# Kernel optimization log

Hardware: AMD Instinct MI355X
Metric: run time of the kernel (lower is better)

The kernel has to match this reference:

```python
import jax, jax.numpy as jnp
import numpy as np

NUM_HEADS = 16


def setup_inputs() -> dict:
    key = jax.random.key(0)
    k0, k1, k2, k3 = jax.random.split(key, 4)
    S, dim = 8192, 1280              # packed vision tokens, embed dim
    H = NUM_HEADS
    D = dim // H                      # head_dim = 80
    n_seg = 8                         # 8 images x 1024 patches
    L = S // n_seg
    return {
        "hidden_states": jax.random.normal(k0, (S, dim), jnp.float32),
        "rotary_pos_emb": jax.random.normal(k1, (S, D // 2), jnp.float32),
        "w_qkv": jax.random.normal(k2, (3 * dim, dim), jnp.float32) * 0.02,
        "b_qkv": jnp.zeros((3 * dim,), jnp.float32),
        "w_proj": jax.random.normal(k3, (dim, dim), jnp.float32) * 0.02,
        "b_proj": jnp.zeros((dim,), jnp.float32),
        "cu_seqlens": jnp.arange(n_seg + 1, dtype=jnp.int32) * L,
    }


def _rotate_half(x):
    x1, x2 = jnp.split(x, 2, axis=-1)
    return jnp.concatenate([-x2, x1], axis=-1)


def _apply_rope(t, freqs):
    # t: [S, H, D]; freqs: [S, D//2]. Matches cat+rotate_half formulation
    # (cos/sin repeated to full head_dim), computed in float32.
    emb = jnp.concatenate([freqs, freqs], axis=-1)          # [S, D]
    cos = jnp.cos(emb)[:, None, :]                          # [S, 1, D]
    sin = jnp.sin(emb)[:, None, :]
    return t * cos + _rotate_half(t) * sin


def reference(hidden_states, rotary_pos_emb, w_qkv, b_qkv, w_proj, b_proj, cu_seqlens):
    S, dim = hidden_states.shape
    H = NUM_HEADS
    D = dim // H
    n_seg = cu_seqlens.shape[0] - 1   # equal-length packed segments
    L = S // n_seg

    qkv = hidden_states @ w_qkv.T + b_qkv                   # [S, 3*dim]
    q, k, v = jnp.split(qkv, 3, axis=-1)
    q = q.reshape(S, H, D)
    k = k.reshape(S, H, D)
    v = v.reshape(S, H, D)

    q = _apply_rope(q, rotary_pos_emb)
    k = _apply_rope(k, rotary_pos_emb)

    # block-diagonal varlen attention: batch over segments instead of an
    # [S, S] dense mask (honors the cu_seqlens sparsity structure)
    qs = q.reshape(n_seg, L, H, D)
    ks = k.reshape(n_seg, L, H, D)
    vs = v.reshape(n_seg, L, H, D)
    scale = D ** -0.5
    scores = jnp.einsum('blhd,bthd->bhlt', qs, ks) * scale  # [n_seg, H, L, L]
    probs = jax.nn.softmax(scores, axis=-1)
    ctx = jnp.einsum('bhlt,bthd->blhd', probs, vs)          # [n_seg, L, H, D]
    ctx = ctx.reshape(S, dim)

    return ctx @ w_proj.T + b_proj                          # [S, dim]
```

## Files before the change

### kernel.cpp

```cpp
#include <hip/hip_runtime.h>
#include <hip/hip_bf16.h>
#include <math.h>

#define S_TOK   8192
#define DIM     1280
#define NHEAD   16
#define HDIM    80
#define NSEG    8
#define SEGLEN  1024
#define QKV_LD  3840
#define DPAD    96

typedef __attribute__((ext_vector_type(8))) short bf16x8;
typedef __attribute__((ext_vector_type(4))) float f32x4;

__device__ __forceinline__ short f2b(float x) {
  __hip_bfloat16 h = __float2bfloat16(x);
  return *reinterpret_cast<short*>(&h);
}
__device__ __forceinline__ float b2f(short x) {
  __hip_bfloat16 h;
  *reinterpret_cast<short*>(&h) = x;
  return __bfloat162float(h);
}

__device__ __forceinline__ void gl_lds16(const void* g, void* l) {
  __builtin_amdgcn_global_load_lds(
      (const __attribute__((address_space(1))) unsigned int*)g,
      (__attribute__((address_space(3))) unsigned int*)l, 16, 0, 0);
}

__global__ __launch_bounds__(256) void cast_f32_bf16(
    const float* __restrict__ in, short* __restrict__ out, int n4)
{
  const int i = blockIdx.x * 256 + threadIdx.x;
  if (i >= n4) return;
  const float4 v = ((const float4*)in)[i];
  short4 o;
  o.x = f2b(v.x); o.y = f2b(v.y); o.z = f2b(v.z); o.w = f2b(v.w);
  ((short4*)out)[i] = o;
}

template<bool OUT_BF16>
__global__ __launch_bounds__(256) void gemm_mfma_nt(
    const short* __restrict__ A, const short* __restrict__ B,
    const float* __restrict__ bias, void* __restrict__ Cout,
    int M, int N, int K)
{
  __shared__ short As[128 * 32];
  __shared__ short Bs[128 * 32];
  const int t = threadIdx.x;
  const int wave = t >> 6, lane = t & 63;
  const int q = lane >> 4, r = lane & 15;
  const int bm = blockIdx.y * 128, bn = blockIdx.x * 128;
  const int wr = (wave >> 1) * 64, wc = (wave & 1) * 64;

  f32x4 acc[4][4];
#pragma unroll
  for (int i = 0; i < 4; ++i)
#pragma unroll
    for (int j = 0; j < 4; ++j) acc[i][j] = (f32x4)(0.f);

  for (int k0 = 0; k0 < K; k0 += 32) {
    __syncthreads();
#pragma unroll
    for (int i = 0; i < 2; ++i) {
      const int c = i * 256 + t;
      const int row = c >> 2, off = (c & 3) * 8;
      gl_lds16(A + (size_t)(bm + row) * K + k0 + off, As + c * 8);
      gl_lds16(B + (size_t)(bn + row) * K + k0 + off, Bs + c * 8);
    }
    __syncthreads();

    bf16x8 af[4], bg[4];
#pragma unroll
    for (int mt = 0; mt < 4; ++mt)
      af[mt] = *(const bf16x8*)&As[(wr + mt * 16 + r) * 32 + q * 8];
#pragma unroll
    for (int nt = 0; nt < 4; ++nt)
      bg[nt] = *(const bf16x8*)&Bs[(wc + nt * 16 + r) * 32 + q * 8];
#pragma unroll
    for (int mt = 0; mt < 4; ++mt)
#pragma unroll
      for (int nt = 0; nt < 4; ++nt)
        acc[mt][nt] = __builtin_amdgcn_mfma_f32_16x16x32_bf16(
            af[mt], bg[nt], acc[mt][nt], 0, 0, 0);
  }

#pragma unroll
  for (int mt = 0; mt < 4; ++mt)
#pragma unroll
    for (int nt = 0; nt < 4; ++nt)
#pragma unroll
      for (int reg = 0; reg < 4; ++reg) {
        const int mrow = bm + wr + mt * 16 + q * 4 + reg;
        const int ncol = bn + wc + nt * 16 + r;
        const float v = acc[mt][nt][reg] + bias[ncol];
        if (OUT_BF16)
          ((short*)Cout)[(size_t)mrow * N + ncol] = f2b(v);
        else
          ((float*)Cout)[(size_t)mrow * N + ncol] = v;
      }
}

__global__ __launch_bounds__(256) void rope_cast(
    const short* __restrict__ qkvb, const float* __restrict__ rot,
    short* __restrict__ Qb, short* __restrict__ Kb)
{
  const int idx = blockIdx.x * 256 + threadIdx.x;
  const int j = idx % 48;
  const int h = (idx / 48) % NHEAD;
  const int s = idx / (48 * NHEAD);
  short* qo = Qb + ((size_t)s * NHEAD + h) * DPAD;
  short* ko = Kb + ((size_t)s * NHEAD + h) * DPAD;
  if (j < 40) {
    const float f = rot[s * 40 + j];
    const float c = cosf(f), sn = sinf(f);
    const short* qi = qkvb + (size_t)s * QKV_LD + h * HDIM;
    const short* ki = qi + DIM;
    const float scale = 0.11180339887498949f;
    const float q0 = b2f(qi[j]), q1 = b2f(qi[j + 40]);
    qo[j]      = f2b((q0 * c - q1 * sn) * scale);
    qo[j + 40] = f2b((q1 * c + q0 * sn) * scale);
    const float k0 = b2f(ki[j]), k1 = b2f(ki[j + 40]);
    ko[j]      = f2b(k0 * c - k1 * sn);
    ko[j + 40] = f2b(k1 * c + k0 * sn);
  } else {
    const int z = 80 + (j - 40);
    qo[z] = 0; qo[z + 8] = 0;
    ko[z] = 0; ko[z + 8] = 0;
  }
}

#define LQK 104
#define LVT 72
#define LPR 72

__global__ __launch_bounds__(256) void attn_mfma(
    const short* __restrict__ Qb, const short* __restrict__ Kb,
    const short* __restrict__ qkvb, short* __restrict__ ctxb)
{
  __shared__ short Qs[64 * LQK];
  __shared__ short Ks[64 * LQK];
  __shared__ short Vt[80 * LVT];
  __shared__ short Ps[4][16 * LPR];

  const int t = threadIdx.x;
  const int wave = t >> 6, lane = t & 63;
  const int q = lane >> 4, r = lane & 15;
  const int seg = blockIdx.z, head = blockIdx.y;
  const int m0 = blockIdx.x * 64;
  const size_t srow0 = (size_t)seg * SEGLEN;

#pragma unroll
  for (int i = 0; i < 3; ++i) {
    const int c = i * 256 + t;
    const int row = c / 12, off = (c % 12) * 8;
    *(bf16x8*)&Qs[row * LQK + off] =
        *(const bf16x8*)(Qb + ((srow0 + m0 + row) * NHEAD + head) * DPAD + off);
  }
  __syncthreads();
  bf16x8 qf[3];
#pragma unroll
  for (int ks = 0; ks < 3; ++ks)
    qf[ks] = *(const bf16x8*)&Qs[(wave * 16 + r) * LQK + ks * 32 + q * 8];

  float m_[4], l_[4];
  f32x4 o[5];
#pragma unroll
  for (int i = 0; i < 4; ++i) { m_[i] = -1e30f; l_[i] = 0.f; }
#pragma unroll
  for (int i = 0; i < 5; ++i) o[i] = (f32x4)(0.f);

  for (int n0 = 0; n0 < SEGLEN; n0 += 64) {
    __syncthreads();
#pragma unroll
    for (int i = 0; i < 3; ++i) {
      const int c = i * 256 + t;
      const int row = c / 12, off = (c % 12) * 8;
      *(bf16x8*)&Ks[row * LQK + off] =
          *(const bf16x8*)(Kb + ((srow0 + n0 + row) * NHEAD + head) * DPAD + off);
    }
#pragma unroll
    for (int i = 0; i < 3; ++i) {
      const int c = i * 256 + t;
      if (c < 640) {
        const int kv = c / 10, c0 = (c % 10) * 8;
        bf16x8 v = *(const bf16x8*)(qkvb + (srow0 + n0 + kv) * QKV_LD +
                                    2 * DIM + head * HDIM + c0);
#pragma unroll
        for (int jj = 0; jj < 8; ++jj)
          Vt[(c0 + jj) * LVT + kv] = v[jj];
      }
    }
    __syncthreads();

    f32x4 s[4];
#pragma unroll
    for (int nt = 0; nt < 4; ++nt) s[nt] = (f32x4)(0.f);
#pragma unroll
    for (int ks = 0; ks < 3; ++ks)
#pragma unroll
      for (int nt = 0; nt < 4; ++nt) {
        bf16x8 kf = *(const bf16x8*)&Ks[(nt * 16 + r) * LQK + ks * 32 + q * 8];
        s[nt] = __builtin_amdgcn_mfma_f32_16x16x32_bf16(qf[ks], kf, s[nt], 0, 0, 0);
      }

#pragma unroll
    for (int reg = 0; reg < 4; ++reg) {
      float sm = fmaxf(fmaxf(s[0][reg], s[1][reg]), fmaxf(s[2][reg], s[3][reg]));
#pragma unroll
      for (int off = 1; off < 16; off <<= 1)
        sm = fmaxf(sm, __shfl_xor(sm, off));
      const float mn = fmaxf(m_[reg], sm);
      const float corr = __expf(m_[reg] - mn);
      m_[reg] = mn;
      float ps = 0.f;
#pragma unroll
      for (int nt = 0; nt < 4; ++nt) {
        const float e = __expf(s[nt][reg] - mn);
        s[nt][reg] = e;
        ps += e;
      }
#pragma unroll
      for (int off = 1; off < 16; off <<= 1)
        ps += __shfl_xor(ps, off);
      l_[reg] = l_[reg] * corr + ps;
#pragma unroll
      for (int dt = 0; dt < 5; ++dt) o[dt][reg] *= corr;
    }

#pragma unroll
    for (int nt = 0; nt < 4; ++nt)
#pragma unroll
      for (int reg = 0; reg < 4; ++reg)
        Ps[wave][(q * 4 + reg) * LPR + nt * 16 + r] = f2b(s[nt][reg]);

#pragma unroll
    for (int ks2 = 0; ks2 < 2; ++ks2) {
      bf16x8 pf = *(const bf16x8*)&Ps[wave][r * LPR + ks2 * 32 + q * 8];
#pragma unroll
      for (int dt = 0; dt < 5; ++dt) {
        bf16x8 vf = *(const bf16x8*)&Vt[(dt * 16 + r) * LVT + ks2 * 32 + q * 8];
        o[dt] = __builtin_amdgcn_mfma_f32_16x16x32_bf16(pf, vf, o[dt], 0, 0, 0);
      }
    }
  }

#pragma unroll
  for (int reg = 0; reg < 4; ++reg) {
    const float inv = 1.f / l_[reg];
    const size_t row = srow0 + m0 + wave * 16 + q * 4 + reg;
#pragma unroll
    for (int dt = 0; dt < 5; ++dt)
      ctxb[row * DIM + head * HDIM + dt * 16 + r] = f2b(o[dt][reg] * inv);
  }
}

extern "C" void kernel_launch(void* const* d_in, const int* in_sizes, int n_in,
                              void* d_out, int out_size, void* d_ws, size_t ws_size,
                              hipStream_t stream)
{
  const float* hs    = (const float*)d_in[0];
  const float* rot   = (const float*)d_in[1];
  const float* wqkv  = (const float*)d_in[2];
  const float* bqkv  = (const float*)d_in[3];
  const float* wproj = (const float*)d_in[4];
  const float* bproj = (const float*)d_in[5];
  float* out = (float*)d_out;

  char* w = (char*)d_ws;
  short* hs_b    = (short*)w;  w += (size_t)S_TOK * DIM * 2;
  short* wqkv_b  = (short*)w;  w += (size_t)QKV_LD * DIM * 2;
  short* wproj_b = (short*)w;  w += (size_t)DIM * DIM * 2;
  short* qkv_b   = (short*)w;  w += (size_t)S_TOK * QKV_LD * 2;
  short* Qb      = (short*)w;  w += (size_t)S_TOK * NHEAD * DPAD * 2;
  short* Kb      = (short*)w;  w += (size_t)S_TOK * NHEAD * DPAD * 2;
  short* ctx_b   = (short*)w;  w += (size_t)S_TOK * DIM * 2;

  dim3 blk(256);

  cast_f32_bf16<<<dim3(S_TOK * DIM / 4 / 256), blk, 0, stream>>>(hs, hs_b, S_TOK * DIM / 4);
  cast_f32_bf16<<<dim3(QKV_LD * DIM / 4 / 256), blk, 0, stream>>>(wqkv, wqkv_b, QKV_LD * DIM / 4);
  cast_f32_bf16<<<dim3(DIM * DIM / 4 / 256), blk, 0, stream>>>(wproj, wproj_b, DIM * DIM / 4);

  gemm_mfma_nt<true><<<dim3(QKV_LD / 128, S_TOK / 128), blk, 0, stream>>>(
      hs_b, wqkv_b, bqkv, qkv_b, S_TOK, QKV_LD, DIM);

  rope_cast<<<dim3(S_TOK * NHEAD * 48 / 256), blk, 0, stream>>>(qkv_b, rot, Qb, Kb);

  attn_mfma<<<dim3(SEGLEN / 64, NHEAD, NSEG), blk, 0, stream>>>(Qb, Kb, qkv_b, ctx_b);

  gemm_mfma_nt<false><<<dim3(DIM / 128, S_TOK / 128), blk, 0, stream>>>(
      ctx_b, wproj_b, bproj, out, S_TOK, DIM, DIM);
}
```

Baseline: 533.7 us.

## Pre-transpose V globally, prefetch K/V into registers, 128-row Q tiles per block

Adds a separate kernel that writes V transposed per segment/head into the reused hidden-states workspace, so attention loads V tiles with vector stores instead of scattered per-element LDS transposes. The attention kernel now processes 32 query rows per wave (128 per block), keeping Q fragments in registers and reusing each K/V tile across two M tiles. The next K/V tile is prefetched into registers while the current one is computed, and MFMA sections get raised wave priority. Costs are an extra launch plus a global V round trip, higher register pressure with a launch-bound occupancy hint of 3, and half as many blocks.

```diff
diff --git a/kernel.cpp b/kernel.cpp
--- a/kernel.cpp
+++ b/kernel.cpp
@@ -132,129 +132,177 @@
   }
 }
 
+__global__ __launch_bounds__(256) void v_transpose(
+    const short* __restrict__ qkvb, short* __restrict__ Vt)
+{
+  const int tid = blockIdx.x * 256 + threadIdx.x;
+  const int c   = tid >> 13;
+  const int kv  = tid & 8191;
+  const int head = c / 10;
+  const int d0   = (c % 10) * 8;
+  const int seg  = kv >> 10;
+  const bf16x8 v = *(const bf16x8*)(qkvb + (size_t)kv * QKV_LD + 2 * DIM +
+                                    head * HDIM + d0);
+  short* ob = Vt + ((size_t)(seg * NHEAD + head) * HDIM + d0) * SEGLEN + (kv & 1023);
+#pragma unroll
+  for (int j = 0; j < 8; ++j)
+    ob[(size_t)j * SEGLEN] = v[j];
+}
+
 #define LQK 104
 #define LVT 72
 #define LPR 72
-
-__global__ __launch_bounds__(256) void attn_mfma(
+#define NT  16
+
+__global__ __launch_bounds__(256, 3) void attn_mfma(
     const short* __restrict__ Qb, const short* __restrict__ Kb,
-    const short* __restrict__ qkvb, short* __restrict__ ctxb)
-{
-  __shared__ short Qs[64 * LQK];
+    const short* __restrict__ Vtg, short* __restrict__ ctxb)
+{
   __shared__ short Ks[64 * LQK];
-  __shared__ short Vt[80 * LVT];
-  __shared__ short Ps[4][16 * LPR];
+  __shared__ short Vs[80 * LVT];
+  __shared__ short Ps[4][32 * LPR];
 
   const int t = threadIdx.x;
   const int wave = t >> 6, lane = t & 63;
   const int q = lane >> 4, r = lane & 15;
   const int seg = blockIdx.z, head = blockIdx.y;
-  const int m0 = blockIdx.x * 64;
+  const int m0 = blockIdx.x * 128;
   const size_t srow0 = (size_t)seg * SEGLEN;
-
-#pragma unroll
-  for (int i = 0; i < 3; ++i) {
-    const int c = i * 256 + t;
-    const int row = c / 12, off = (c % 12) * 8;
-    *(bf16x8*)&Qs[row * LQK + off] =
-        *(const bf16x8*)(Qb + ((srow0 + m0 + row) * NHEAD + head) * DPAD + off);
-  }
-  __syncthreads();
-  bf16x8 qf[3];
-#pragma unroll
-  for (int ks = 0; ks < 3; ++ks)
-    qf[ks] = *(const bf16x8*)&Qs[(wave * 16 + r) * LQK + ks * 32 + q * 8];
-
-  float m_[4], l_[4];
-  f32x4 o[5];
-#pragma unroll
-  for (int i = 0; i < 4; ++i) { m_[i] = -1e30f; l_[i] = 0.f; }
-#pragma unroll
-  for (int i = 0; i < 5; ++i) o[i] = (f32x4)(0.f);
-
-  for (int n0 = 0; n0 < SEGLEN; n0 += 64) {
+  const size_t vbase = (size_t)(seg * NHEAD + head) * HDIM * SEGLEN;
+
+  bf16x8 qf[2][3];
+#pragma unroll
+  for (int mt = 0; mt < 2; ++mt)
+#pragma unroll
+    for (int ks = 0; ks < 3; ++ks)
+      qf[mt][ks] = *(const bf16x8*)(
+          Qb + ((srow0 + m0 + wave * 32 + mt * 16 + r) * NHEAD + head) * DPAD +
+          ks * 32 + q * 8);
+
+  float m_[2][4], l_[2][4];
+  f32x4 o[2][5];
+#pragma unroll
+  for (int mt = 0; mt < 2; ++mt) {
+#pragma unroll
+    for (int i = 0; i < 4; ++i) { m_[mt][i] = -1e30f; l_[mt][i] = 0.f; }
+#pragma unroll
+    for (int i = 0; i < 5; ++i) o[mt][i] = (f32x4)(0.f);
+  }
+
+  bf16x8 kreg[3], vreg[3];
+  const int kc_row[3] = {(0 * 256 + t) / 12, (1 * 256 + t) / 12, (2 * 256 + t) / 12};
+  const int kc_off[3] = {((0 * 256 + t) % 12) * 8, ((1 * 256 + t) % 12) * 8,
+                         ((2 * 256 + t) % 12) * 8};
+
+#define LOAD_TILE(n0)                                                          \
+  {                                                                            \
+    _Pragma("unroll")                                                          \
+    for (int i = 0; i < 3; ++i)                                                \
+      kreg[i] = *(const bf16x8*)(                                              \
+          Kb + ((srow0 + (n0) + kc_row[i]) * NHEAD + head) * DPAD + kc_off[i]);\
+    _Pragma("unroll")                                                          \
+    for (int i = 0; i < 3; ++i) {                                              \
+      const int c = i * 256 + t;                                               \
+      if (c < 640)                                                             \
+        vreg[i] = *(const bf16x8*)(Vtg + vbase + (size_t)(c >> 3) * SEGLEN +   \
+                                   (n0) + (c & 7) * 8);                        \
+    }                                                                          \
+  }
+
+  LOAD_TILE(0)
+
+  for (int tile = 0; tile < NT; ++tile) {
     __syncthreads();
+#pragma unroll
+    for (int i = 0; i < 3; ++i)
+      *(bf16x8*)&Ks[kc_row[i] * LQK + kc_off[i]] = kreg[i];
 #pragma unroll
     for (int i = 0; i < 3; ++i) {
       const int c = i * 256 + t;
-      const int row = c / 12, off = (c % 12) * 8;
-      *(bf16x8*)&Ks[row * LQK + off] =
-          *(const bf16x8*)(Kb + ((srow0 + n0 + row) * NHEAD + head) * DPAD + off);
+      if (c < 640)
+        *(bf16x8*)&Vs[(c >> 3) * LVT + (c & 7) * 8] = vreg[i];
     }
-#pragma unroll
-    for (int i = 0; i < 3; ++i) {
-      const int c = i * 256 + t;
-      if (c < 640) {
-        const int kv = c / 10, c0 = (c % 10) * 8;
-        bf16x8 v = *(const bf16x8*)(qkvb + (srow0 + n0 + kv) * QKV_LD +
-                                    2 * DIM + head * HDIM + c0);
-#pragma unroll
-        for (int jj = 0; jj < 8; ++jj)
-          Vt[(c0 + jj) * LVT + kv] = v[jj];
+    __syncthreads();
+
+    if (tile + 1 < NT) LOAD_TILE((tile + 1) * 64)
+
+    f32x4 s[2][4];
+#pragma unroll
+    for (int mt = 0; mt < 2; ++mt)
+#pragma unroll
+      for (int nt = 0; nt < 4; ++nt) s[mt][nt] = (f32x4)(0.f);
+    __builtin_amdgcn_s_setprio(1);
+#pragma unroll
+    for (int ks = 0; ks < 3; ++ks)
+#pragma unroll
+      for (int nt = 0; nt < 4; ++nt) {
+        const bf16x8 kf = *(const bf16x8*)&Ks[(nt * 16 + r) * LQK + ks * 32 + q * 8];
+        s[0][nt] = __builtin_amdgcn_mfma_f32_16x16x32_bf16(qf[0][ks], kf, s[0][nt], 0, 0, 0);
+        s[1][nt] = __builtin_amdgcn_mfma_f32_16x16x32_bf16(qf[1][ks], kf, s[1][nt], 0, 0, 0);
+      }
+    __builtin_amdgcn_s_setprio(0);
+
+#pragma unroll
+    for (int mt = 0; mt < 2; ++mt)
+#pragma unroll
+      for (int reg = 0; reg < 4; ++reg) {
+        float sm = fmaxf(fmaxf(s[mt][0][reg], s[mt][1][reg]),
+                         fmaxf(s[mt][2][reg], s[mt][3][reg]));
+#pragma unroll
+        for (int off = 1; off < 16; off <<= 1)
+          sm = fmaxf(sm, __shfl_xor(sm, off));
+        const float mn = fmaxf(m_[mt][reg], sm);
+        const float corr = __expf(m_[mt][reg] - mn);
+        m_[mt][reg] = mn;
+        float ps = 0.f;
+#pragma unroll
+        for (int nt = 0; nt < 4; ++nt) {
+          const float e = __expf(s[mt][nt][reg] - mn);
+          s[mt][nt][reg] = e;
+          ps += e;
+        }
+#pragma unroll
+        for (int off = 1; off < 16; off <<= 1)
+          ps += __shfl_xor(ps, off);
+        l_[mt][reg] = l_[mt][reg] * corr + ps;
+#pragma unroll
+        for (int dt = 0; dt < 5; ++dt) o[mt][dt][reg] *= corr;
+      }
+
+#pragma unroll
+    for (int mt = 0; mt < 2; ++mt)
+#pragma unroll
+      for (int nt = 0; nt < 4; ++nt)
+#pragma unroll
+        for (int reg = 0; reg < 4; ++reg)
+          Ps[wave][(mt * 16 + q * 4 + reg) * LPR + nt * 16 + r] =
+              f2b(s[mt][nt][reg]);
+
+    __builtin_amdgcn_s_setprio(1);
+#pragma unroll
+    for (int ks2 = 0; ks2 < 2; ++ks2) {
+      const bf16x8 pf0 = *(const bf16x8*)&Ps[wave][r * LPR + ks2 * 32 + q * 8];
+      const bf16x8 pf1 = *(const bf16x8*)&Ps[wave][(16 + r) * LPR + ks2 * 32 + q * 8];
+#pragma unroll
+      for (int dt = 0; dt < 5; ++dt) {
+        const bf16x8 vf = *(const bf16x8*)&Vs[(dt * 16 + r) * LVT + ks2 * 32 + q * 8];
+        o[0][dt] = __builtin_amdgcn_mfma_f32_16x16x32_bf16(pf0, vf, o[0][dt], 0, 0, 0);
+        o[1][dt] = __builtin_amdgcn_mfma_f32_16x16x32_bf16(pf1, vf, o[1][dt], 0, 0, 0);
       }
     }
-    __syncthreads();
-
-    f32x4 s[4];
-#pragma unroll
-    for (int nt = 0; nt < 4; ++nt) s[nt] = (f32x4)(0.f);
-#pragma unroll
-    for (int ks = 0; ks < 3; ++ks)
-#pragma unroll
-      for (int nt = 0; nt < 4; ++nt) {
-        bf16x8 kf = *(const bf16x8*)&Ks[(nt * 16 + r) * LQK + ks * 32 + q * 8];
-        s[nt] = __builtin_amdgcn_mfma_f32_16x16x32_bf16(qf[ks], kf, s[nt], 0, 0, 0);
-      }
-
+    __builtin_amdgcn_s_setprio(0);
+  }
+
+#pragma unroll
+  for (int mt = 0; mt < 2; ++mt)
 #pragma unroll
     for (int reg = 0; reg < 4; ++reg) {
-      float sm = fmaxf(fmaxf(s[0][reg], s[1][reg]), fmaxf(s[2][reg], s[3][reg]));
-#pragma unroll
-      for (int off = 1; off < 16; off <<= 1)
-        sm = fmaxf(sm, __shfl_xor(sm, off));
-      const float mn = fmaxf(m_[reg], sm);
-      const float corr = __expf(m_[reg] - mn);
-      m_[reg] = mn;
-      float ps = 0.f;
-#pragma unroll
-      for (int nt = 0; nt < 4; ++nt) {
-        const float e = __expf(s[nt][reg] - mn);
-        s[nt][reg] = e;
-        ps += e;
-      }
-#pragma unroll
-      for (int off = 1; off < 16; off <<= 1)
-        ps += __shfl_xor(ps, off);
-      l_[reg] = l_[reg] * corr + ps;
-#pragma unroll
-      for (int dt = 0; dt < 5; ++dt) o[dt][reg] *= corr;
+      const float inv = 1.f / l_[mt][reg];
+      const size_t row = srow0 + m0 + wave * 32 + mt * 16 + q * 4 + reg;
+#pragma unroll
+      for (int dt = 0; dt < 5; ++dt)
+        ctxb[row * DIM + head * HDIM + dt * 16 + r] = f2b(o[mt][dt][reg] * inv);
     }
-
-#pragma unroll
-    for (int nt = 0; nt < 4; ++nt)
-#pragma unroll
-      for (int reg = 0; reg < 4; ++reg)
-        Ps[wave][(q * 4 + reg) * LPR + nt * 16 + r] = f2b(s[nt][reg]);
-
-#pragma unroll
-    for (int ks2 = 0; ks2 < 2; ++ks2) {
-      bf16x8 pf = *(const bf16x8*)&Ps[wave][r * LPR + ks2 * 32 + q * 8];
-#pragma unroll
-      for (int dt = 0; dt < 5; ++dt) {
-        bf16x8 vf = *(const bf16x8*)&Vt[(dt * 16 + r) * LVT + ks2 * 32 + q * 8];
-        o[dt] = __builtin_amdgcn_mfma_f32_16x16x32_bf16(pf, vf, o[dt], 0, 0, 0);
-      }
-    }
-  }
-
-#pragma unroll
-  for (int reg = 0; reg < 4; ++reg) {
-    const float inv = 1.f / l_[reg];
-    const size_t row = srow0 + m0 + wave * 16 + q * 4 + reg;
-#pragma unroll
-    for (int dt = 0; dt < 5; ++dt)
-      ctxb[row * DIM + head * HDIM + dt * 16 + r] = f2b(o[dt][reg] * inv);
-  }
 }
 
 extern "C" void kernel_launch(void* const* d_in, const int* in_sizes, int n_in,
@@ -277,6 +325,7 @@
   short* Qb      = (short*)w;  w += (size_t)S_TOK * NHEAD * DPAD * 2;
   short* Kb      = (short*)w;  w += (size_t)S_TOK * NHEAD * DPAD * 2;
   short* ctx_b   = (short*)w;  w += (size_t)S_TOK * DIM * 2;
+  short* Vt_g    = hs_b;
 
   dim3 blk(256);
 
@@ -289,7 +338,9 @@
 
   rope_cast<<<dim3(S_TOK * NHEAD * 48 / 256), blk, 0, stream>>>(qkv_b, rot, Qb, Kb);
 
-  attn_mfma<<<dim3(SEGLEN / 64, NHEAD, NSEG), blk, 0, stream>>>(Qb, Kb, qkv_b, ctx_b);
+  v_transpose<<<dim3(160 * S_TOK / 256), blk, 0, stream>>>(qkv_b, Vt_g);
+
+  attn_mfma<<<dim3(SEGLEN / 128, NHEAD, NSEG), blk, 0, stream>>>(Qb, Kb, Vt_g, ctx_b);
 
   gemm_mfma_nt<false><<<dim3(DIM / 128, S_TOK / 128), blk, 0, stream>>>(
       ctx_b, wproj_b, bproj, out, S_TOK, DIM, DIM);
```

New measurement: 523.9 us. Within noise of the previous version (-1.8%).
